# Performance work log

Hardware: AMD Instinct MI355X
Metric: run time of the kernel (lower is better)

The kernel has to match this reference:

```python
import jax, jax.numpy as jnp
import numpy as np

B, N, S, DG, C_IN, C_OUT, HID = 2, 128, 4, 8, 4, 8, 32


def setup_inputs() -> dict:
    key = jax.random.key(0)
    ks = jax.random.split(key, 10)

    def w(k, shape, fan_in):
        return jax.random.normal(k, shape, jnp.float32) / np.float32(np.sqrt(fan_in))

    return {
        "pairwise_g": jax.random.normal(ks[0], (B, N, N, S, S, DG), jnp.float32),
        "coset_functions": jax.random.normal(ks[1], (B, N, S, C_IN), jnp.float32),
        "mask": jax.random.bernoulli(ks[2], 0.9, (B, N, S)),
        "ky_W1": w(ks[3], (C_IN, HID, 2), 2), "ky_b1": jnp.zeros((C_IN, HID), jnp.float32),
        "ky_W2": w(ks[4], (C_IN, HID, HID), HID), "ky_b2": jnp.zeros((C_IN, HID), jnp.float32),
        "ky_W3": w(ks[5], (C_IN, 1, HID), HID), "ky_b3": jnp.zeros((C_IN, 1), jnp.float32),
        "kg_W1": w(ks[6], (C_IN, HID, DG), DG), "kg_b1": jnp.zeros((C_IN, HID), jnp.float32),
        "kg_W2": w(ks[7], (C_IN, HID, HID), HID), "kg_b2": jnp.zeros((C_IN, HID), jnp.float32),
        "kg_W3": w(ks[8], (C_IN, 1, HID), HID), "kg_b3": jnp.zeros((C_IN, 1), jnp.float32),
        "w_out": w(ks[9], (C_OUT, C_IN), C_IN),
    }


def _mlp(x, W1, b1, W2, b2, W3, b3):
    # NerualNetKernel with bn=False, act=Swish: (Linear + SiLU) x 3, incl. output layer.
    h = jax.nn.silu(x @ W1.T + b1)
    h = jax.nn.silu(h @ W2.T + b2)
    return jax.nn.silu(h @ W3.T + b3)


def reference(pairwise_g, coset_functions, mask,
              ky_W1, ky_b1, ky_W2, ky_b2, ky_W3, ky_b3,
              kg_W1, kg_b1, kg_W2, kg_b2, kg_W3, kg_b3, w_out):
    b, n, _, s, _, _ = pairwise_g.shape
    c_in = coset_functions.shape[-1]
    key_mask = mask[:, None, :, None, :, None]  # (B,1,N,1,S,1) masks key points/samples
    outs = []
    for i in range(c_in):  # fixed small channel loop, as in the original module
        f = coset_functions[..., i:i + 1]  # (B,N,S,1)
        y1 = jnp.broadcast_to(f[:, None, :, None, :, :], (b, n, n, s, s, 1))  # key side
        y2 = jnp.broadcast_to(f[:, :, None, :, None, :], (b, n, n, s, s, 1))  # query side
        y = jnp.concatenate([y1, y2], axis=-1)  # (B,N,N,S,S,2)
        k = (_mlp(y, ky_W1[i], ky_b1[i], ky_W2[i], ky_b2[i], ky_W3[i], ky_b3[i])
             + _mlp(pairwise_g, kg_W1[i], kg_b1[i], kg_W2[i], kg_b2[i], kg_W3[i], kg_b3[i]))
        att = jnp.where(key_mask, jnp.exp(k), jnp.zeros((), k.dtype))  # (B,N,N,S,S,1)
        att = att / att.sum(axis=(2, 4), keepdims=True)
        f = f + (att * f[:, None, :, None, :, :]).sum(axis=(2, 4))  # residual + weighted agg
        outs.append(f)
    cf = jnp.concatenate(outs, axis=-1)  # (B,N,S,C_IN)
    cf = cf * mask[..., None].astype(cf.dtype)
    return cf @ w_out.T  # (B,N,S,C_OUT), bias-free output transform
```

## Files before the change

### kernel.cpp

```cpp
#include <hip/hip_runtime.h>
#include <hip/hip_bf16.h>

#define BB   2
#define NN   128
#define SS   4
#define DGG  8
#define CIN  4
#define COUT 8
#define HH   32
#define NT   256

#define SCN  (-1.44269504f)

typedef __attribute__((ext_vector_type(4))) float          fvec4;
typedef __attribute__((ext_vector_type(4))) unsigned short usvec4;
typedef __attribute__((ext_vector_type(8))) unsigned short usvec8;
typedef __attribute__((ext_vector_type(2))) __fp16         half2v;
typedef __attribute__((ext_vector_type(8))) __fp16         f16x8;
typedef __attribute__((ext_vector_type(4))) float          f32x4;
typedef __attribute__((ext_vector_type(4))) unsigned int   uvec4;

__device__ __forceinline__ float bf2f(unsigned short u) {
    return __uint_as_float(((unsigned int)u) << 16);
}
__device__ __forceinline__ float sil_u(float u) {
    float e = __builtin_amdgcn_exp2f(u);
    return u * __builtin_amdgcn_rcpf(1.0f + e);
}

__device__ __forceinline__ unsigned int pk2u(float a, float b) {
#if __has_builtin(__builtin_amdgcn_cvt_pkrtz)
    half2v h = __builtin_amdgcn_cvt_pkrtz(a, b);
#else
    half2v h; h[0] = (__fp16)a; h[1] = (__fp16)b;
#endif
    union { half2v h; unsigned int u; } x; x.h = h; return x.u;
}
union FU { uvec4 u; f16x8 h; };
__device__ __forceinline__ f16x8 mk_frag(unsigned a, unsigned b, unsigned c, unsigned d) {
    FU x; x.u = (uvec4){a, b, c, d}; return x.h;
}
__device__ __forceinline__ f16x8 mk_fragv(uvec4 u) {
    FU x; x.u = u; return x.h;
}
__device__ __forceinline__ f16x8 sil_frag(f32x4 a, f32x4 b) {
    return mk_frag(pk2u(sil_u(a[0]), sil_u(a[1])),
                   pk2u(sil_u(a[2]), sil_u(a[3])),
                   pk2u(sil_u(b[0]), sil_u(b[1])),
                   pk2u(sil_u(b[2]), sil_u(b[3])));
}

__device__ __forceinline__ float loadS(const void* p, int idx, int fmode) {
    return fmode ? bf2f(((const unsigned short*)p)[idx])
                 : ((const float*)p)[idx];
}
__device__ __forceinline__ void load8(const void* p, int base, int fmode, float* dst) {
    if (fmode) {
        usvec8 v = *(const usvec8*)((const unsigned short*)p + base);
#pragma unroll
        for (int d = 0; d < 8; ++d) dst[d] = bf2f(v[d]);
    } else {
        fvec4 a = *(const fvec4*)((const float*)p + base);
        fvec4 b = *(const fvec4*)((const float*)p + base + 4);
        dst[0] = a[0]; dst[1] = a[1]; dst[2] = a[2]; dst[3] = a[3];
        dst[4] = b[0]; dst[5] = b[1]; dst[6] = b[2]; dst[7] = b[3];
    }
}
__device__ __forceinline__ int load_mask(const void* p, int idx, int mmode) {
    if (mmode == 0) return ((const int*)p)[idx] != 0;
    if (mmode == 1) return ((const unsigned short*)p)[idx] != 0;
    if (mmode == 2) return ((const unsigned char*)p)[idx] != 0;
    return ((const unsigned int*)p)[idx] != 0;
}
__device__ __forceinline__ void stage_pk(unsigned int* dst, const void* src,
                                         int pairs, int fmode, int tid, float sc) {
    if (fmode) {
        const unsigned short* s = (const unsigned short*)src;
        for (int x = tid; x < pairs; x += NT)
            dst[x] = pk2u(sc * bf2f(s[2 * x]), sc * bf2f(s[2 * x + 1]));
    } else {
        const float* s = (const float*)src;
        for (int x = tid; x < pairs; x += NT)
            dst[x] = pk2u(sc * s[2 * x], sc * s[2 * x + 1]);
    }
}
__device__ __forceinline__ void copy_arr(float* sm, const void* src, int off,
                                         int cnt, int fmode, int tid, float sc) {
    if (fmode) {
        const unsigned short* s = (const unsigned short*)src;
        for (int x = tid; x < cnt; x += NT) sm[off + x] = sc * bf2f(s[x]);
    } else {
        const float* s = (const float*)src;
        for (int x = tid; x < cnt; x += NT) sm[off + x] = sc * s[x];
    }
}
__device__ __forceinline__ void detect_inline(const void* g_mask, const void* g_coset,
                                              int tid, int* smi, int slot) {
    if (tid < 64) {
        const unsigned short* cu = (const unsigned short*)g_coset;
        unsigned short v = cu[2 * tid];
        int e = (v >> 7) & 0xFF;
        int hits = __popcll(__ballot(e >= 110 && e <= 135));
        int fmode_ = (hits > 32) ? 1 : 0;
        const unsigned short* mu = (const unsigned short*)g_mask;
        int evenBF = 0, any3 = 0, anyByte = 0;
        for (int r = 0; r < 8; ++r) {
            int idx = tid + r * 64;
            unsigned short m = mu[idx];
            if (m == 0x3F80) { any3 = 1; if (!(idx & 1)) evenBF = 1; }
            if (m == 0x0101 || m == 0x0100) anyByte = 1;
        }
        evenBF  = (__ballot(evenBF)  != 0ull);
        any3    = (__ballot(any3)    != 0ull);
        anyByte = (__ballot(anyByte) != 0ull);
        if (tid == 0) {
            smi[slot]     = fmode_;
            smi[slot + 1] = evenBF ? 1 : (any3 ? 3 : (anyByte ? 2 : 0));
        }
    }
}

#define UG_G    0
#define F_FA    2048
#define U_YW1n  4096
#define U_GW1   4608
#define U_GB1q  5120
#define U_W2Y   5632
#define U_W2G   7680
#define F_YB2   9728
#define F_GB2   9856
#define U_YW3   9984
#define U_GW3   10048
#define F_YB3   10112
#define F_GB3   10116
#define U_CB1   10120
#define F_RED   10128
#define F_MODE  10160
#define U_TOTAL 10162

__global__ __launch_bounds__(NT, 4) void emha_mfma(
    const void* __restrict__ g_pw, const void* __restrict__ g_coset,
    const void* __restrict__ g_mask,
    const void* yW1, const void* yb1, const void* yW2, const void* yb2,
    const void* yW3, const void* yb3,
    const void* gW1, const void* gb1, const void* gW2, const void* gb2,
    const void* gW3, const void* gb3,
    const void* wout, void* outp)
{
    __shared__ __align__(16) unsigned int smu[U_TOTAL];
    float* smf = (float*)smu;
    int*   smi = (int*)smu;
    const int tid = threadIdx.x;

    detect_inline(g_mask, g_coset, tid, smi, F_MODE);
    __syncthreads();
    const int fmode = smi[F_MODE];
    const int mmode = smi[F_MODE + 1];
    __syncthreads();

    const int bn = blockIdx.x >> 2;
    const int s1 = blockIdx.x & 3;
    const int b  = bn >> 7;
    const int n1 = bn & 127;

#pragma unroll
    for (int it = 0; it < 2; ++it) {
        const int pos = tid + it * 256;
        const int n2 = pos >> 2, s2 = pos & 3;
        float g8[8];
        load8(g_pw, (((bn * NN + n2) * SS + s1) * SS + s2) * DGG, fmode, g8);
#pragma unroll
        for (int q = 0; q < 4; ++q)
            smu[UG_G + pos * 4 + q] = pk2u(g8[2 * q], g8[2 * q + 1]);
    }
    for (int x = tid; x < 2048; x += NT)
        smf[F_FA + x] = loadS(g_coset, b * 2048 + x, fmode);
    for (int x = tid; x < 128; x += NT) {
        smu[U_YW1n + x * 4 + 0] = pk2u(SCN * loadS(yW1, 2 * x, fmode),
                                       SCN * loadS(yW1, 2 * x + 1, fmode));
        smu[U_YW1n + x * 4 + 1] = pk2u(SCN * loadS(yb1, x, fmode), 0.f);
        smu[U_YW1n + x * 4 + 2] = 0u;
        smu[U_YW1n + x * 4 + 3] = 0u;
        smu[U_GB1q + x * 4 + 0] = pk2u(SCN * loadS(gb1, x, fmode), 0.f);
        smu[U_GB1q + x * 4 + 1] = 0u;
        smu[U_GB1q + x * 4 + 2] = 0u;
        smu[U_GB1q + x * 4 + 3] = 0u;
    }
    stage_pk(&smu[U_GW1], gW1, 512,  fmode, tid, SCN);
    stage_pk(&smu[U_W2Y], yW2, 2048, fmode, tid, 1.0f);
    stage_pk(&smu[U_W2G], gW2, 2048, fmode, tid, 1.0f);
    stage_pk(&smu[U_YW3], yW3, 64,   fmode, tid, 1.0f);
    stage_pk(&smu[U_GW3], gW3, 64,   fmode, tid, 1.0f);
    copy_arr(smf, yb2, F_YB2, 128, fmode, tid, SCN);
    copy_arr(smf, gb2, F_GB2, 128, fmode, tid, SCN);
    copy_arr(smf, yb3, F_YB3, 4, fmode, tid, SCN);
    copy_arr(smf, gb3, F_GB3, 4, fmode, tid, SCN);
    if (tid < 8) smu[U_CB1 + tid] = (tid == 0) ? 0x00003C00u : 0u;

    const int lane = tid & 63;
    const int wave = tid >> 6;
    const int mLo = load_mask(g_mask, b * 512 + wave * 128 + lane, mmode);
    const int mHi = load_mask(g_mask, b * 512 + wave * 128 + 64 + lane, mmode);
    const unsigned long long kmL = __ballot(mLo != 0);
    const unsigned long long kmH = __ballot(mHi != 0);
    __syncthreads();

    const int quad = lane >> 4;
    const int col  = lane & 15;
    const int qpos = n1 * 4 + s1;
    const int h0   = ((col >> 2) << 3) + (col & 3);
    const unsigned* Zp = &smu[U_CB1 + 4];
    const f32x4 zf = {0.f, 0.f, 0.f, 0.f};

#pragma unroll 1
    for (int ci = 0; ci < CIN; ++ci) {
        const int rowy = (ci * 32 + h0) * 4;
        const f16x8 AY1a = mk_fragv(*(const uvec4*)((quad == 0) ? &smu[U_YW1n + rowy] : Zp));
        const f16x8 AY1b = mk_fragv(*(const uvec4*)((quad == 0) ? &smu[U_YW1n + rowy + 16] : Zp));
        const f16x8 GA = mk_fragv(*(const uvec4*)((quad == 0) ? &smu[U_GW1 + rowy]
                                   : (quad == 1) ? &smu[U_GB1q + rowy] : Zp));
        const f16x8 GB = mk_fragv(*(const uvec4*)((quad == 0) ? &smu[U_GW1 + rowy + 16]
                                   : (quad == 1) ? &smu[U_GB1q + rowy + 16] : Zp));
        const f16x8 Ay0 = mk_fragv(*(const uvec4*)&smu[U_W2Y + ci * 512 + h0 * 16 + quad * 4]);
        const f16x8 Ay1 = mk_fragv(*(const uvec4*)&smu[U_W2Y + ci * 512 + (h0 + 4) * 16 + quad * 4]);
        const f16x8 Ag0 = mk_fragv(*(const uvec4*)&smu[U_W2G + ci * 512 + h0 * 16 + quad * 4]);
        const f16x8 Ag1 = mk_fragv(*(const uvec4*)&smu[U_W2G + ci * 512 + (h0 + 4) * 16 + quad * 4]);
        const fvec4 cY0 = *(const fvec4*)&smf[F_YB2 + ci * 32 + quad * 8];
        const fvec4 cY1 = *(const fvec4*)&smf[F_YB2 + ci * 32 + quad * 8 + 4];
        const fvec4 cG0 = *(const fvec4*)&smf[F_GB2 + ci * 32 + quad * 8];
        const fvec4 cG1 = *(const fvec4*)&smf[F_GB2 + ci * 32 + quad * 8 + 4];
        const f16x8 A3y = mk_fragv(*(const uvec4*)((col == 0) ? &smu[U_YW3 + ci * 16 + quad * 4] : Zp));
        const f16x8 A3g = mk_fragv(*(const uvec4*)((col == 0) ? &smu[U_GW3 + ci * 16 + quad * 4] : Zp));

        const float fb  = smf[F_FA + qpos * 4 + ci];
        const float b3y = smf[F_YB3 + ci];
        const float b3g = smf[F_GB3 + ci];

        const unsigned* pBg = (quad == 0) ? &smu[UG_G + (wave * 128 + col) * 4]
                            : ((quad == 1) ? &smu[U_CB1] : Zp);
        const int stepBg = (quad == 0) ? 64 : 0;
        const float* pFA = &smf[F_FA + (wave * 128 + col) * 4 + ci];

        float fap_c = *pFA;
        f32x4 d1a, d1b, dga, dgb;
        {
            const uvec4 gq0 = *(const uvec4*)pBg;
            const f16x8 Bg1 = mk_fragv(gq0);
            const f16x8 B1y = mk_frag(pk2u(fap_c, fb), 0x00003C00u, 0u, 0u);
#if defined(__HIP_DEVICE_COMPILE__)
            d1a = __builtin_amdgcn_mfma_f32_16x16x32_f16(AY1a, B1y, zf, 0, 0, 0);
            d1b = __builtin_amdgcn_mfma_f32_16x16x32_f16(AY1b, B1y, zf, 0, 0, 0);
            dga = __builtin_amdgcn_mfma_f32_16x16x32_f16(GA,   Bg1, zf, 0, 0, 0);
            dgb = __builtin_amdgcn_mfma_f32_16x16x32_f16(GB,   Bg1, zf, 0, 0, 0);
#else
            d1a = zf; d1b = zf; dga = zf; dgb = zf;
#endif
        }

        float aN = 0.f, aD = 0.f;
#pragma unroll 1
        for (int t = 0; t < 8; ++t) {
            pBg += stepBg;
            pFA += 64;
            const uvec4 gqn = *(const uvec4*)pBg;
            const float fapn = *pFA;

            const f16x8 By = sil_frag(d1a, d1b);
            const f16x8 Bg = sil_frag(dga, dgb);

            {
                const f16x8 Bg1n = mk_fragv(gqn);
                const f16x8 B1yn = mk_frag(pk2u(fapn, fb), 0x00003C00u, 0u, 0u);
#if defined(__HIP_DEVICE_COMPILE__)
                d1a = __builtin_amdgcn_mfma_f32_16x16x32_f16(AY1a, B1yn, zf, 0, 0, 0);
                d1b = __builtin_amdgcn_mfma_f32_16x16x32_f16(AY1b, B1yn, zf, 0, 0, 0);
                dga = __builtin_amdgcn_mfma_f32_16x16x32_f16(GA,   Bg1n, zf, 0, 0, 0);
                dgb = __builtin_amdgcn_mfma_f32_16x16x32_f16(GB,   Bg1n, zf, 0, 0, 0);
#else
                d1a = zf; d1b = zf; dga = zf; dgb = zf;
#endif
            }

            f32x4 dy0, dy1, dg0, dg1, dy3, dg3;
#if defined(__HIP_DEVICE_COMPILE__)
            dy0 = __builtin_amdgcn_mfma_f32_16x16x32_f16(Ay0, By, cY0, 0, 0, 0);
            dy1 = __builtin_amdgcn_mfma_f32_16x16x32_f16(Ay1, By, cY1, 0, 0, 0);
            dg0 = __builtin_amdgcn_mfma_f32_16x16x32_f16(Ag0, Bg, cG0, 0, 0, 0);
            dg1 = __builtin_amdgcn_mfma_f32_16x16x32_f16(Ag1, Bg, cG1, 0, 0, 0);
#else
            dy0 = cY0; dy1 = cY1; dg0 = cG0; dg1 = cG1;
#endif
            const f16x8 By2 = sil_frag(dy0, dy1);
            const f16x8 Bg2 = sil_frag(dg0, dg1);

#if defined(__HIP_DEVICE_COMPILE__)
            dy3 = __builtin_amdgcn_mfma_f32_16x16x32_f16(A3y, By2, zf, 0, 0, 0);
            dg3 = __builtin_amdgcn_mfma_f32_16x16x32_f16(A3g, Bg2, zf, 0, 0, 0);
#else
            dy3 = zf; dg3 = zf;
#endif
            const float v3y = sil_u(dy3[0] + b3y);
            const float v3g = sil_u(dg3[0] + b3g);
            const unsigned long long sel = (t < 4) ? kmL : kmH;
            const int kb = (int)((sel >> (((t & 3) << 4) + col)) & 1);
            const float e = kb ? __builtin_amdgcn_exp2f(-(v3y + v3g)) : 0.f;
            aD += e;
            aN += e * fap_c;

            fap_c = fapn;
        }
        aN += __shfl_xor(aN, 1);  aD += __shfl_xor(aD, 1);
        aN += __shfl_xor(aN, 2);  aD += __shfl_xor(aD, 2);
        aN += __shfl_xor(aN, 4);  aD += __shfl_xor(aD, 4);
        aN += __shfl_xor(aN, 8);  aD += __shfl_xor(aD, 8);
        if (lane == 0) {
            smf[F_RED + (wave * 4 + ci) * 2 + 0] = aN;
            smf[F_RED + (wave * 4 + ci) * 2 + 1] = aD;
        }
    }
    __syncthreads();

    if (tid < COUT) {
        const int o = tid;
        const int m1 = load_mask(g_mask, b * 512 + qpos, mmode);
        float acc = 0.f;
#pragma unroll
        for (int ci = 0; ci < CIN; ++ci) {
            float N = 0.f, D = 0.f;
#pragma unroll
            for (int w = 0; w < 4; ++w) {
                N += smf[F_RED + (w * 4 + ci) * 2 + 0];
                D += smf[F_RED + (w * 4 + ci) * 2 + 1];
            }
            const float fbv = smf[F_FA + qpos * 4 + ci];
            const float cf = m1 ? (fbv + N / D) : 0.f;
            acc += cf * loadS(wout, o * CIN + ci, fmode);
        }
        const int oidx = (bn * SS + s1) * COUT + o;
        if (fmode) ((__hip_bfloat16*)outp)[oidx] = __float2bfloat16(acc);
        else       ((float*)outp)[oidx] = acc;
    }
}

extern "C" void kernel_launch(void* const* d_in, const int* in_sizes, int n_in,
                              void* d_out, int out_size, void* d_ws, size_t ws_size,
                              hipStream_t stream) {
    emha_mfma<<<BB * NN * SS, NT, 0, stream>>>(
        d_in[0], d_in[1], d_in[2],
        d_in[3], d_in[4], d_in[5], d_in[6], d_in[7], d_in[8],
        d_in[9], d_in[10], d_in[11], d_in[12], d_in[13], d_in[14],
        d_in[15], d_out);
}
```

Baseline: 160.1 us.

## Deepen MFMA software pipeline to three stages across MLP layers

```diff
diff --git a/kernel.cpp b/kernel.cpp
--- a/kernel.cpp
+++ b/kernel.cpp
@@ -241,17 +241,44 @@
         const int stepBg = (quad == 0) ? 64 : 0;
         const float* pFA = &smf[F_FA + (wave * 128 + col) * 4 + ci];
 
-        float fap_c = *pFA;
+        float fap0 = *pFA;
+        f32x4 r2y0, r2y1, r2g0, r2g1;
         f32x4 d1a, d1b, dga, dgb;
         {
             const uvec4 gq0 = *(const uvec4*)pBg;
-            const f16x8 Bg1 = mk_fragv(gq0);
-            const f16x8 B1y = mk_frag(pk2u(fap_c, fb), 0x00003C00u, 0u, 0u);
-#if defined(__HIP_DEVICE_COMPILE__)
-            d1a = __builtin_amdgcn_mfma_f32_16x16x32_f16(AY1a, B1y, zf, 0, 0, 0);
-            d1b = __builtin_amdgcn_mfma_f32_16x16x32_f16(AY1b, B1y, zf, 0, 0, 0);
-            dga = __builtin_amdgcn_mfma_f32_16x16x32_f16(GA,   Bg1, zf, 0, 0, 0);
-            dgb = __builtin_amdgcn_mfma_f32_16x16x32_f16(GB,   Bg1, zf, 0, 0, 0);
+            const f16x8 Bg10 = mk_fragv(gq0);
+            const f16x8 B1y0 = mk_frag(pk2u(fap0, fb), 0x00003C00u, 0u, 0u);
+            f32x4 t1a, t1b, tga, tgb;
+#if defined(__HIP_DEVICE_COMPILE__)
+            t1a = __builtin_amdgcn_mfma_f32_16x16x32_f16(AY1a, B1y0, zf, 0, 0, 0);
+            t1b = __builtin_amdgcn_mfma_f32_16x16x32_f16(AY1b, B1y0, zf, 0, 0, 0);
+            tga = __builtin_amdgcn_mfma_f32_16x16x32_f16(GA,   Bg10, zf, 0, 0, 0);
+            tgb = __builtin_amdgcn_mfma_f32_16x16x32_f16(GB,   Bg10, zf, 0, 0, 0);
+#else
+            t1a = zf; t1b = zf; tga = zf; tgb = zf;
+#endif
+            const f16x8 By0 = sil_frag(t1a, t1b);
+            const f16x8 Bg0 = sil_frag(tga, tgb);
+#if defined(__HIP_DEVICE_COMPILE__)
+            r2y0 = __builtin_amdgcn_mfma_f32_16x16x32_f16(Ay0, By0, cY0, 0, 0, 0);
+            r2y1 = __builtin_amdgcn_mfma_f32_16x16x32_f16(Ay1, By0, cY1, 0, 0, 0);
+            r2g0 = __builtin_amdgcn_mfma_f32_16x16x32_f16(Ag0, Bg0, cG0, 0, 0, 0);
+            r2g1 = __builtin_amdgcn_mfma_f32_16x16x32_f16(Ag1, Bg0, cG1, 0, 0, 0);
+#else
+            r2y0 = cY0; r2y1 = cY1; r2g0 = cG0; r2g1 = cG1;
+#endif
+        }
+        pBg += stepBg; pFA += 64;
+        float fap1 = *pFA;
+        {
+            const uvec4 gq1 = *(const uvec4*)pBg;
+            const f16x8 Bg11 = mk_fragv(gq1);
+            const f16x8 B1y1 = mk_frag(pk2u(fap1, fb), 0x00003C00u, 0u, 0u);
+#if defined(__HIP_DEVICE_COMPILE__)
+            d1a = __builtin_amdgcn_mfma_f32_16x16x32_f16(AY1a, B1y1, zf, 0, 0, 0);
+            d1b = __builtin_amdgcn_mfma_f32_16x16x32_f16(AY1b, B1y1, zf, 0, 0, 0);
+            dga = __builtin_amdgcn_mfma_f32_16x16x32_f16(GA,   Bg11, zf, 0, 0, 0);
+            dgb = __builtin_amdgcn_mfma_f32_16x16x32_f16(GB,   Bg11, zf, 0, 0, 0);
 #else
             d1a = zf; d1b = zf; dga = zf; dgb = zf;
 #endif
@@ -262,37 +289,12 @@
         for (int t = 0; t < 8; ++t) {
             pBg += stepBg;
             pFA += 64;
-            const uvec4 gqn = *(const uvec4*)pBg;
-            const float fapn = *pFA;
-
-            const f16x8 By = sil_frag(d1a, d1b);
-            const f16x8 Bg = sil_frag(dga, dgb);
-
-            {
-                const f16x8 Bg1n = mk_fragv(gqn);
-                const f16x8 B1yn = mk_frag(pk2u(fapn, fb), 0x00003C00u, 0u, 0u);
-#if defined(__HIP_DEVICE_COMPILE__)
-                d1a = __builtin_amdgcn_mfma_f32_16x16x32_f16(AY1a, B1yn, zf, 0, 0, 0);
-                d1b = __builtin_amdgcn_mfma_f32_16x16x32_f16(AY1b, B1yn, zf, 0, 0, 0);
-                dga = __builtin_amdgcn_mfma_f32_16x16x32_f16(GA,   Bg1n, zf, 0, 0, 0);
-                dgb = __builtin_amdgcn_mfma_f32_16x16x32_f16(GB,   Bg1n, zf, 0, 0, 0);
-#else
-                d1a = zf; d1b = zf; dga = zf; dgb = zf;
-#endif
-            }
-
-            f32x4 dy0, dy1, dg0, dg1, dy3, dg3;
-#if defined(__HIP_DEVICE_COMPILE__)
-            dy0 = __builtin_amdgcn_mfma_f32_16x16x32_f16(Ay0, By, cY0, 0, 0, 0);
-            dy1 = __builtin_amdgcn_mfma_f32_16x16x32_f16(Ay1, By, cY1, 0, 0, 0);
-            dg0 = __builtin_amdgcn_mfma_f32_16x16x32_f16(Ag0, Bg, cG0, 0, 0, 0);
-            dg1 = __builtin_amdgcn_mfma_f32_16x16x32_f16(Ag1, Bg, cG1, 0, 0, 0);
-#else
-            dy0 = cY0; dy1 = cY1; dg0 = cG0; dg1 = cG1;
-#endif
-            const f16x8 By2 = sil_frag(dy0, dy1);
-            const f16x8 Bg2 = sil_frag(dg0, dg1);
-
+            const uvec4 gq2 = *(const uvec4*)pBg;
+            const float fap2 = *pFA;
+
+            const f16x8 By2 = sil_frag(r2y0, r2y1);
+            const f16x8 Bg2 = sil_frag(r2g0, r2g1);
+            f32x4 dy3, dg3;
 #if defined(__HIP_DEVICE_COMPILE__)
             dy3 = __builtin_amdgcn_mfma_f32_16x16x32_f16(A3y, By2, zf, 0, 0, 0);
             dg3 = __builtin_amdgcn_mfma_f32_16x16x32_f16(A3g, Bg2, zf, 0, 0, 0);
@@ -305,9 +307,34 @@
             const int kb = (int)((sel >> (((t & 3) << 4) + col)) & 1);
             const float e = kb ? __builtin_amdgcn_exp2f(-(v3y + v3g)) : 0.f;
             aD += e;
-            aN += e * fap_c;
-
-            fap_c = fapn;
+            aN += e * fap0;
+
+            const f16x8 By = sil_frag(d1a, d1b);
+            const f16x8 Bg = sil_frag(dga, dgb);
+#if defined(__HIP_DEVICE_COMPILE__)
+            r2y0 = __builtin_amdgcn_mfma_f32_16x16x32_f16(Ay0, By, cY0, 0, 0, 0);
+            r2y1 = __builtin_amdgcn_mfma_f32_16x16x32_f16(Ay1, By, cY1, 0, 0, 0);
+            r2g0 = __builtin_amdgcn_mfma_f32_16x16x32_f16(Ag0, Bg, cG0, 0, 0, 0);
+            r2g1 = __builtin_amdgcn_mfma_f32_16x16x32_f16(Ag1, Bg, cG1, 0, 0, 0);
+#else
+            r2y0 = cY0; r2y1 = cY1; r2g0 = cG0; r2g1 = cG1;
+#endif
+
+            {
+                const f16x8 Bg1n = mk_fragv(gq2);
+                const f16x8 B1yn = mk_frag(pk2u(fap2, fb), 0x00003C00u, 0u, 0u);
+#if defined(__HIP_DEVICE_COMPILE__)
+                d1a = __builtin_amdgcn_mfma_f32_16x16x32_f16(AY1a, B1yn, zf, 0, 0, 0);
+                d1b = __builtin_amdgcn_mfma_f32_16x16x32_f16(AY1b, B1yn, zf, 0, 0, 0);
+                dga = __builtin_amdgcn_mfma_f32_16x16x32_f16(GA,   Bg1n, zf, 0, 0, 0);
+                dgb = __builtin_amdgcn_mfma_f32_16x16x32_f16(GB,   Bg1n, zf, 0, 0, 0);
+#else
+                d1a = zf; d1b = zf; dga = zf; dgb = zf;
+#endif
+            }
+
+            fap0 = fap1;
+            fap1 = fap2;
         }
         aN += __shfl_xor(aN, 1);  aD += __shfl_xor(aD, 1);
         aN += __shfl_xor(aN, 2);  aD += __shfl_xor(aD, 2);
```

Result: no change. 162.0 us (+1.2%).
